# Kernel tuning notes

Measured on AMD Instinct MI355X. Metric: run time of the kernel, lower is better.

The kernel has to match this reference:

```python
import jax, jax.numpy as jnp
import numpy as np

EPS = 1e-5

def _rms(t, w):
    # RMSNorm over last dim with learned scale w (broadcastable)
    return t * jax.lax.rsqrt(jnp.mean(t * t, axis=-1, keepdims=True) + EPS) * w

def setup_inputs() -> dict:
    key = jax.random.key(0)
    ks = jax.random.split(key, 8)
    B, S, D, H, HD, M = 2, 2048, 1024, 16, 64, 2
    E = H * HD
    sc = 0.02
    x = jax.random.normal(ks[0], (B, S, D), jnp.float32)
    attn_mask = jnp.zeros((S, S), jnp.float32)  # additive mask
    mod_ids = jax.random.randint(ks[1], (B, S), 0, M)
    Wq = jax.random.normal(ks[2], (M, D, E), jnp.float32) * sc
    Wk = jax.random.normal(ks[3], (M, D, E), jnp.float32) * sc
    Wv = jax.random.normal(ks[4], (M, D, E), jnp.float32) * sc
    Wo = jax.random.normal(ks[5], (M, E, D), jnp.float32) * sc
    qn_w = jnp.ones((M, HD), jnp.float32)
    kn_w = jnp.ones((M, HD), jnp.float32)
    attn_norm_w = jnp.ones((M, D), jnp.float32)
    return {"x": x, "attn_mask": attn_mask, "mod_ids": mod_ids,
            "Wq": Wq, "Wk": Wk, "Wv": Wv, "Wo": Wo,
            "qn_w": qn_w, "kn_w": kn_w, "attn_norm_w": attn_norm_w}

def reference(x, attn_mask, mod_ids, Wq, Wk, Wv, Wo, qn_w, kn_w, attn_norm_w):
    B, S, D = x.shape
    M = Wq.shape[0]
    HD = qn_w.shape[-1]
    E = Wq.shape[-1]
    H = E // HD
    msk = jax.nn.one_hot(mod_ids, M, dtype=x.dtype)  # [B,S,M] one-hot routing

    # modality-expert QKV projections: [M,B,S,E]
    q_m = jnp.einsum('bsd,mde->mbse', x, Wq).reshape(M, B, S, H, HD)
    k_m = jnp.einsum('bsd,mde->mbse', x, Wk).reshape(M, B, S, H, HD)
    v_m = jnp.einsum('bsd,mde->mbse', x, Wv)
    # per-modality, per-head QK RMSNorm
    q_m = _rms(q_m, qn_w[:, None, None, None, :]).reshape(M, B, S, E)
    k_m = _rms(k_m, kn_w[:, None, None, None, :]).reshape(M, B, S, E)

    # merge modalities (scatter by routing mask)
    q = jnp.einsum('bsm,mbse->bse', msk, q_m).reshape(B, S, H, HD)
    k = jnp.einsum('bsm,mbse->bse', msk, k_m).reshape(B, S, H, HD)
    v = jnp.einsum('bsm,mbse->bse', msk, v_m).reshape(B, S, H, HD)

    # standard multi-head attention
    scores = jnp.einsum('bqhd,bkhd->bhqk', q, k) / jnp.sqrt(jnp.asarray(HD, x.dtype))
    scores = scores + attn_mask  # additive mask broadcast over [B,H]
    attn = jax.nn.softmax(scores, axis=-1)
    ctx = jnp.einsum('bhqk,bkhd->bqhd', attn, v).reshape(B, S, E)
    attn_weights = attn.mean(axis=1)  # [B,S,S], averaged over heads

    # modality-expert output projection + RMSNorm, scatter-merge back
    o_m = jnp.einsum('bse,med->mbsd', ctx, Wo)
    o_m = _rms(o_m, attn_norm_w[:, None, None, :])
    out = jnp.einsum('bsm,mbsd->bsd', msk, o_m)
    return out, attn_weights
```

## Files before the change

kernel.cpp:

```cpp
#include <hip/hip_runtime.h>
#include <cstdint>

#define Bc  2
#define Sc  2048
#define Dc  1024
#define Ec  1024
#define Hc  16
#define HDc 64
#define TTc (Bc*Sc)
#define TILE_R 128
#define NTILES 36
#define EPSc 1e-5f
#define LOG2E 1.44269504f
#define C2    (0.125f*LOG2E)

typedef unsigned short u16;
using bf8   = __attribute__((ext_vector_type(8))) short;
using f32x4 = __attribute__((ext_vector_type(4))) float;
#define MFMA(a,b,c) __builtin_amdgcn_mfma_f32_16x16x32_bf16(a,b,c,0,0,0)

static __device__ __forceinline__ u16 f2b(float f){
    return (u16)((__float_as_uint(f) + 0x8000u) >> 16);
}
static __device__ __forceinline__ float b2f(u16 s){
    return __uint_as_float(((unsigned)s) << 16);
}
static __device__ __forceinline__ unsigned cvtpk(float a, float b){
    unsigned r;
    asm("v_cvt_pk_bf16_f32 %0, %1, %2" : "=v"(r) : "v"(a), "v"(b));
    return r;
}
union bfpack { unsigned u[4]; bf8 v; };
static __device__ __forceinline__ u16* swz(u16* base, int row, int col8){
    return base + row*64 + ((col8 ^ (row & 7)) << 3);
}
static __device__ __forceinline__ const u16* swzc(const u16* base, int row, int col8){
    return base + row*64 + ((col8 ^ (row & 7)) << 3);
}

__global__ void k_perm(const int* __restrict__ mod, int* __restrict__ perm,
                       int* __restrict__ tmeta)
{
    __shared__ int cnt[4], segstart[4];
    int t = threadIdx.x;
    if (t < 4) cnt[t] = 0;
    __syncthreads();
    for (int i = t; i < TTc; i += 256){
        int b = i >> 11; int m = mod[i];
        atomicAdd(&cnt[b*2+m], 1);
    }
    __syncthreads();
    if (t == 0){
        int off = 0;
        for (int i = 0; i < 4; i++){
            segstart[i] = off;
            int pad = ((cnt[i] + TILE_R - 1)/TILE_R)*TILE_R;
            for (int tt = off/TILE_R; tt < (off+pad)/TILE_R; tt++) tmeta[tt] = i;
            off += pad;
        }
        for (int tt = off/TILE_R; tt < NTILES; tt++) tmeta[tt] = -1;
    }
    __syncthreads();
    if (t < 4) cnt[t] = 0;
    for (int i = t; i < NTILES*TILE_R; i += 256) perm[i] = -1;
    __syncthreads();
    for (int i = t; i < TTc; i += 256){
        int b = i >> 11, s = i & 2047; int m = mod[i];
        int r = atomicAdd(&cnt[b*2+m], 1);
        perm[segstart[b*2+m] + r] = s;
    }
}

__global__ __launch_bounds__(256) void k_f2b(const float* __restrict__ src,
                                             u16* __restrict__ dst, int n)
{
    int i = (blockIdx.x*256 + threadIdx.x)*4;
    if (i >= n) return;
    float4 v = *(const float4*)&src[i];
    ushort4 o;
    o.x = f2b(v.x); o.y = f2b(v.y); o.z = f2b(v.z); o.w = f2b(v.w);
    *(ushort4*)&dst[i] = o;
}

__global__ __launch_bounds__(256) void k_f2bs(const float* __restrict__ src,
                                              u16* __restrict__ dst, int n, float sc)
{
    int i = (blockIdx.x*256 + threadIdx.x)*4;
    if (i >= n) return;
    float4 v = *(const float4*)&src[i];
    ushort4 o;
    o.x = f2b(v.x*sc); o.y = f2b(v.y*sc); o.z = f2b(v.z*sc); o.w = f2b(v.w*sc);
    *(ushort4*)&dst[i] = o;
}

__global__ __launch_bounds__(256) void k_tcvt(
    const float* __restrict__ s0, const float* __restrict__ s1,
    const float* __restrict__ s2, const float* __restrict__ s3,
    u16* __restrict__ d0, u16* __restrict__ d1,
    u16* __restrict__ d2, u16* __restrict__ d3)
{
    int wsel = blockIdx.z >> 1, m = blockIdx.z & 1;
    const float* src = (wsel==0?s0:wsel==1?s1:wsel==2?s2:s3) + (size_t)m*1048576;
    u16*       dst = (wsel==0?d0:wsel==1?d1:wsel==2?d2:d3) + (size_t)m*1048576;
    __shared__ float sh[32][33];
    int t = threadIdx.x;
    int i0 = blockIdx.x*32, j0 = blockIdx.y*32;
    {
        int i = t >> 3, j4 = (t & 7)*4;
        *(float4*)&sh[i][j4] = *(const float4*)&src[(size_t)(i0+i)*1024 + j0 + j4];
    }
    __syncthreads();
    {
        int j = t >> 3, i4 = (t & 7)*4;
        ushort4 o;
        o.x = f2b(sh[i4+0][j]); o.y = f2b(sh[i4+1][j]);
        o.z = f2b(sh[i4+2][j]); o.w = f2b(sh[i4+3][j]);
        *(ushort4*)&dst[(size_t)(j0+j)*1024 + i0 + i4] = o;
    }
}

__global__ __launch_bounds__(256) void k_qkv(
    const u16* __restrict__ xb, const u16* __restrict__ wqT,
    const u16* __restrict__ wkT, const u16* __restrict__ wvT,
    const int* __restrict__ perm, const int* __restrict__ tmeta,
    const float* __restrict__ qnw, const float* __restrict__ knw,
    u16* __restrict__ qb, u16* __restrict__ kb, u16* __restrict__ vb)
{
    int meta = tmeta[blockIdx.y];
    if (meta < 0) return;
    int b = meta >> 1, m = meta & 1;
    const u16* W = (blockIdx.z==0 ? wqT : (blockIdx.z==1 ? wkT : wvT)) + (size_t)m*Ec*Dc;
    u16* outp    = (blockIdx.z==0 ? qb  : (blockIdx.z==1 ? kb  : vb));
    int c0 = blockIdx.x*128;
    int t = threadIdx.x, lane = t & 63, wv_ = t >> 6;
    int quad = lane >> 4, lc = lane & 15;

    __shared__ u16 at[128*64];
    __shared__ u16 bt[128*64];
    __shared__ int sperm[128];
    if (t < 128) sperm[t] = perm[blockIdx.y*128 + t];
    f32x4 acc[2][8];
    #pragma unroll
    for (int i=0;i<2;i++)
        #pragma unroll
        for (int j=0;j<8;j++) acc[i][j] = (f32x4){0.f,0.f,0.f,0.f};
    __syncthreads();

    int rr = t >> 1, hf = t & 1;
    for (int d0 = 0; d0 < Dc; d0 += 64){
        int s_ = sperm[rr];
        if (s_ >= 0){
            const u16* src = xb + ((size_t)(b*Sc + s_))*Dc + d0 + hf*32;
            *(uint4*)swz(at, rr, hf*4+0) = *(const uint4*)(src);
            *(uint4*)swz(at, rr, hf*4+1) = *(const uint4*)(src + 8);
            *(uint4*)swz(at, rr, hf*4+2) = *(const uint4*)(src + 16);
            *(uint4*)swz(at, rr, hf*4+3) = *(const uint4*)(src + 24);
        } else {
            uint4 z = make_uint4(0,0,0,0);
            *(uint4*)swz(at, rr, hf*4+0) = z;
            *(uint4*)swz(at, rr, hf*4+1) = z;
            *(uint4*)swz(at, rr, hf*4+2) = z;
            *(uint4*)swz(at, rr, hf*4+3) = z;
        }
        const u16* wsrc = W + (size_t)(c0 + rr)*Dc + d0 + hf*32;
        *(uint4*)swz(bt, rr, hf*4+0) = *(const uint4*)(wsrc);
        *(uint4*)swz(bt, rr, hf*4+1) = *(const uint4*)(wsrc + 8);
        *(uint4*)swz(bt, rr, hf*4+2) = *(const uint4*)(wsrc + 16);
        *(uint4*)swz(bt, rr, hf*4+3) = *(const uint4*)(wsrc + 24);
        __syncthreads();
        #pragma unroll
        for (int ks = 0; ks < 2; ks++){
            bf8 a0 = *(const bf8*)swzc(at, wv_*32 + lc,      ks*4 + quad);
            bf8 a1 = *(const bf8*)swzc(at, wv_*32 + 16 + lc, ks*4 + quad);
            #pragma unroll
            for (int nb = 0; nb < 8; nb++){
                bf8 bb = *(const bf8*)swzc(bt, nb*16 + lc, ks*4 + quad);
                acc[0][nb] = MFMA(a0, bb, acc[0][nb]);
                acc[1][nb] = MFMA(a1, bb, acc[1][nb]);
            }
        }
        __syncthreads();
    }

    if (blockIdx.z < 2){
        const float* nw = (blockIdx.z==0 ? qnw : knw) + m*HDc;
        float cs = (blockIdx.z==0) ? C2 : 1.f;
        float w0 = nw[lc]*cs, w1 = nw[16+lc]*cs, w2 = nw[32+lc]*cs, w3 = nw[48+lc]*cs;
        #pragma unroll
        for (int mb = 0; mb < 2; mb++){
            #pragma unroll
            for (int r = 0; r < 4; r++){
                #pragma unroll
                for (int g = 0; g < 2; g++){
                    float ss = 0.f;
                    #pragma unroll
                    for (int j = 0; j < 4; j++){
                        float v2 = acc[mb][g*4+j][r];
                        ss += v2*v2;
                    }
                    ss += __shfl_xor(ss, 1, 64);
                    ss += __shfl_xor(ss, 2, 64);
                    ss += __shfl_xor(ss, 4, 64);
                    ss += __shfl_xor(ss, 8, 64);
                    float rs = rsqrtf(ss*(1.f/64.f) + EPSc);
                    acc[mb][g*4+0][r] *= rs*w0;
                    acc[mb][g*4+1][r] *= rs*w1;
                    acc[mb][g*4+2][r] *= rs*w2;
                    acc[mb][g*4+3][r] *= rs*w3;
                }
            }
        }
    }

    int h0 = c0 >> 6;
    #pragma unroll
    for (int mb = 0; mb < 2; mb++){
        #pragma unroll
        for (int r = 0; r < 4; r++){
            int row = wv_*32 + mb*16 + quad*4 + r;
            int s_ = sperm[row];
            if (s_ < 0) continue;
            #pragma unroll
            for (int nb = 0; nb < 8; nb++){
                int col = nb*16 + lc;
                int h = h0 + (col >> 6), hd = col & 63;
                outp[(((size_t)(b*Hc + h))*Sc + s_)*HDc + hd] = f2b(acc[mb][nb][r]);
            }
        }
    }
}

__global__ __launch_bounds__(256) void k_vt(const u16* __restrict__ vb,
                                            u16* __restrict__ vtb)
{
    __shared__ u16 sh[64][72];
    int t = threadIdx.x;
    int s0 = blockIdx.x*64, bh = blockIdx.y;
    {
        int rr = t >> 2, cc = (t & 3)*16;
        const u16* src = vb + ((size_t)bh*Sc + s0 + rr)*HDc + cc;
        *(uint4*)&sh[rr][cc]   = *(const uint4*)(src);
        *(uint4*)&sh[rr][cc+8] = *(const uint4*)(src+8);
    }
    __syncthreads();
    {
        int hd = t >> 2, sc = (t & 3)*16;
        u16 tmp[16];
        #pragma unroll
        for (int j = 0; j < 16; j++) tmp[j] = sh[sc+j][hd];
        u16* dst = vtb + ((size_t)bh*HDc + hd)*Sc + s0 + sc;
        *(uint4*)(dst)   = *(const uint4*)&tmp[0];
        *(uint4*)(dst+8) = *(const uint4*)&tmp[8];
    }
}

__global__ __launch_bounds__(256) void k_flash(
    const u16* __restrict__ qb, const u16* __restrict__ kb,
    const u16* __restrict__ vtb, const u16* __restrict__ maskb,
    float* __restrict__ pm, float* __restrict__ pl,
    u16* __restrict__ c0, u16* __restrict__ c1)
{
    int qs0 = blockIdx.x*64, h = blockIdx.y;
    int b = blockIdx.z >> 1, half = blockIdx.z & 1;
    u16* ctxh = half ? c1 : c0;
    int t = threadIdx.x, lane = t & 63, wv_ = t >> 6;
    int quad = lane >> 4, lc = lane & 15;
    __shared__ u16 kt[64*64];
    __shared__ u16 vt[64*64];
    const u16* qp  = qb  + ((size_t)(b*Hc+h))*Sc*HDc;
    const u16* kp  = kb  + ((size_t)(b*Hc+h))*Sc*HDc;
    const u16* vtp = vtb + ((size_t)(b*Hc+h))*HDc*Sc;
    const u16* mq  = maskb + (size_t)(qs0 + wv_*16 + lc)*Sc;
    bf8 aq[2];
    #pragma unroll
    for (int ks = 0; ks < 2; ks++)
        aq[ks] = *(const bf8*)(qp + (size_t)(qs0 + wv_*16 + lc)*HDc + ks*32 + quad*8);
    float rm = -1.0e30f, rl = 0.f;
    f32x4 oacc[4];
    #pragma unroll
    for (int j=0;j<4;j++) oacc[j] = (f32x4){0.f,0.f,0.f,0.f};

    int rr = t >> 2, c8 = (t & 3)*2;
    int pr = (rr & 0x23) | ((rr & 0x04) << 2) | ((rr & 0x18) >> 1);
    int kc0 = half*1024;
    for (int kc = kc0; kc < kc0 + 1024; kc += 64){
        ushort4 mv[2][2];
        #pragma unroll
        for (int a1 = 0; a1 < 2; a1++)
            #pragma unroll
            for (int b1 = 0; b1 < 2; b1++)
                mv[a1][b1] = *(const ushort4*)(mq + kc + a1*32 + quad*8 + b1*4);
        __syncthreads();
        {
            const u16* s1 = kp + (size_t)(kc+rr)*HDc + c8*8;
            *(uint4*)swz(kt, pr, c8)   = *(const uint4*)(s1);
            *(uint4*)swz(kt, pr, c8+1) = *(const uint4*)(s1+8);
            const u16* s2 = vtp + (size_t)rr*Sc + kc + c8*8;
            *(uint4*)swz(vt, rr, c8)   = *(const uint4*)(s2);
            *(uint4*)swz(vt, rr, c8+1) = *(const uint4*)(s2+8);
        }
        __syncthreads();
        f32x4 acc[4];
        #pragma unroll
        for (int j=0;j<4;j++) acc[j] = (f32x4){0.f,0.f,0.f,0.f};
        #pragma unroll
        for (int ks = 0; ks < 2; ks++){
            #pragma unroll
            for (int nb = 0; nb < 4; nb++){
                bf8 ak = *(const bf8*)swzc(kt, nb*16 + lc, ks*4 + quad);
                acc[nb] = MFMA(ak, aq[ks], acc[nb]);
            }
        }
        float sv[4][4];
        float mxl = -3.0e38f;
        #pragma unroll
        for (int a1 = 0; a1 < 2; a1++){
            #pragma unroll
            for (int b1 = 0; b1 < 2; b1++){
                int nb = 2*a1 + b1;
                #pragma unroll
                for (int r = 0; r < 4; r++){
                    u16 mraw = (r==0?mv[a1][b1].x:r==1?mv[a1][b1].y:
                                r==2?mv[a1][b1].z:mv[a1][b1].w);
                    float s2v = acc[nb][r] + b2f(mraw);
                    sv[nb][r] = s2v;
                    mxl = fmaxf(mxl, s2v);
                }
            }
        }
        if (__any(mxl > rm + 8.f)){
            float mx = fmaxf(mxl, __shfl_xor(mxl, 16, 64));
            mx = fmaxf(mx, __shfl_xor(mx, 32, 64));
            float nm = fmaxf(rm, mx);
            float fac = exp2f(rm - nm);
            rm = nm;
            rl *= fac;
            float f0 = __shfl(fac, quad*4+0, 64);
            float f1 = __shfl(fac, quad*4+1, 64);
            float f2 = __shfl(fac, quad*4+2, 64);
            float f3 = __shfl(fac, quad*4+3, 64);
            #pragma unroll
            for (int nb = 0; nb < 4; nb++){
                oacc[nb][0] *= f0; oacc[nb][1] *= f1;
                oacc[nb][2] *= f2; oacc[nb][3] *= f3;
            }
        }
        #pragma unroll
        for (int a1 = 0; a1 < 2; a1++){
            bfpack pk;
            {
                float p0 = exp2f(sv[2*a1][0] - rm);
                float p1 = exp2f(sv[2*a1][1] - rm);
                float p2 = exp2f(sv[2*a1][2] - rm);
                float p3 = exp2f(sv[2*a1][3] - rm);
                rl += (p0 + p1) + (p2 + p3);
                pk.u[0] = cvtpk(p0, p1); pk.u[1] = cvtpk(p2, p3);
            }
            {
                float p0 = exp2f(sv[2*a1+1][0] - rm);
                float p1 = exp2f(sv[2*a1+1][1] - rm);
                float p2 = exp2f(sv[2*a1+1][2] - rm);
                float p3 = exp2f(sv[2*a1+1][3] - rm);
                rl += (p0 + p1) + (p2 + p3);
                pk.u[2] = cvtpk(p0, p1); pk.u[3] = cvtpk(p2, p3);
            }
            bf8 ap = pk.v;
            #pragma unroll
            for (int nb2 = 0; nb2 < 4; nb2++){
                bf8 bv = *(const bf8*)swzc(vt, nb2*16 + lc, a1*4 + quad);
                oacc[nb2] = MFMA(ap, bv, oacc[nb2]);
            }
        }
    }
    rl += __shfl_xor(rl, 16, 64);
    rl += __shfl_xor(rl, 32, 64);
    if (quad == 0){
        size_t srow = ((size_t)(b*Hc+h))*Sc + qs0 + wv_*16 + lc;
        pm[(size_t)half*65536 + srow] = rm;
        pl[(size_t)half*65536 + srow] = rl;
    }
    float i0 = 1.f/__shfl(rl, quad*4+0, 64);
    float i1 = 1.f/__shfl(rl, quad*4+1, 64);
    float i2 = 1.f/__shfl(rl, quad*4+2, 64);
    float i3 = 1.f/__shfl(rl, quad*4+3, 64);
    #pragma unroll
    for (int r = 0; r < 4; r++){
        float ir = (r==0?i0:r==1?i1:r==2?i2:i3);
        int tok = qs0 + wv_*16 + quad*4 + r;
        #pragma unroll
        for (int nb = 0; nb < 4; nb++){
            int hd = nb*16 + lc;
            ctxh[((size_t)(b*Sc + tok))*Ec + h*HDc + hd] = f2b(oacc[nb][r]*ir);
        }
    }
}

__global__ __launch_bounds__(256) void k_merge(
    const float* __restrict__ pm, const float* __restrict__ pl,
    float* __restrict__ lstc, float* __restrict__ w0, float* __restrict__ w1)
{
    int r = blockIdx.x*256 + threadIdx.x;
    float m0 = pm[r],        m1 = pm[65536 + r];
    float l0 = pl[r],        l1 = pl[65536 + r];
    float M  = fmaxf(m0, m1);
    float e0 = exp2f(m0 - M)*l0;
    float e1 = exp2f(m1 - M)*l1;
    float L  = e0 + e1;
    float iL = 1.f/L;
    lstc[r] = M + log2f(L);
    w0[r] = e0*iL;
    w1[r] = e1*iL;
}

__global__ __launch_bounds__(256) void k_addc(u16* __restrict__ c0,
                                              const u16* __restrict__ c1,
                                              const float* __restrict__ w0,
                                              const float* __restrict__ w1)
{
    int i = (blockIdx.x*256 + threadIdx.x)*8;
    int hh = (i >> 6) & 15, s = (i >> 10) & 2047, bb = i >> 21;
    int wi = ((bb*Hc + hh) << 11) + s;
    float wa = w0[wi], wb = w1[wi];
    ushort4 a0 = *(ushort4*)&c0[i],   a1 = *(ushort4*)&c0[i+4];
    ushort4 b0 = *(const ushort4*)&c1[i], b1 = *(const ushort4*)&c1[i+4];
    ushort4 o0, o1;
    o0.x = f2b(b2f(a0.x)*wa + b2f(b0.x)*wb); o0.y = f2b(b2f(a0.y)*wa + b2f(b0.y)*wb);
    o0.z = f2b(b2f(a0.z)*wa + b2f(b0.z)*wb); o0.w = f2b(b2f(a0.w)*wa + b2f(b0.w)*wb);
    o1.x = f2b(b2f(a1.x)*wa + b2f(b1.x)*wb); o1.y = f2b(b2f(a1.y)*wa + b2f(b1.y)*wb);
    o1.z = f2b(b2f(a1.z)*wa + b2f(b1.z)*wb); o1.w = f2b(b2f(a1.w)*wa + b2f(b1.w)*wb);
    *(ushort4*)&c0[i]   = o0;
    *(ushort4*)&c0[i+4] = o1;
}

__global__ __launch_bounds__(256) void k_attnw(
    const u16* __restrict__ qb, const u16* __restrict__ kb,
    const u16* __restrict__ maskb, const float* __restrict__ lstc,
    float* __restrict__ awout)
{
    int qs0 = blockIdx.x*64, ks0 = blockIdx.y*64, b = blockIdx.z;
    int t = threadIdx.x, lane = t & 63, wv_ = t >> 6;
    int quad = lane >> 4, lc = lane & 15;
    __shared__ u16 kt[64*64];
    __shared__ float scc[64];
    f32x4 T[4];
    #pragma unroll
    for (int j=0;j<4;j++) T[j] = (f32x4){0.f,0.f,0.f,0.f};

    for (int h = 0; h < Hc; h++){
        __syncthreads();
        const u16* qp = qb + ((size_t)(b*Hc+h))*Sc*HDc;
        const u16* kp = kb + ((size_t)(b*Hc+h))*Sc*HDc;
        bf8 aq[2];
        #pragma unroll
        for (int ks = 0; ks < 2; ks++)
            aq[ks] = *(const bf8*)(qp + (size_t)(qs0 + wv_*16 + lc)*HDc + ks*32 + quad*8);
        {
            int rr = t >> 2, c8 = (t & 3)*2;
            const u16* s2 = kp + (size_t)(ks0+rr)*HDc + c8*8;
            *(uint4*)swz(kt, rr, c8)   = *(const uint4*)(s2);
            *(uint4*)swz(kt, rr, c8+1) = *(const uint4*)(s2+8);
        }
        if (t < 64)
            scc[t] = lstc[((size_t)(b*Hc+h))*Sc + qs0 + t];
        __syncthreads();
        f32x4 acc[4];
        #pragma unroll
        for (int j=0;j<4;j++) acc[j] = (f32x4){0.f,0.f,0.f,0.f};
        #pragma unroll
        for (int ks = 0; ks < 2; ks++){
            #pragma unroll
            for (int nb = 0; nb < 4; nb++){
                bf8 bb = *(const bf8*)swzc(kt, nb*16 + lc, ks*4 + quad);
                acc[nb] = MFMA(aq[ks], bb, acc[nb]);
            }
        }
        #pragma unroll
        for (int r = 0; r < 4; r++){
            int row = wv_*16 + quad*4 + r;
            float cv = scc[row];
            #pragma unroll
            for (int nb = 0; nb < 4; nb++)
                T[nb][r] += exp2f(acc[nb][r] - cv);
        }
    }
    #pragma unroll
    for (int r = 0; r < 4; r++){
        int gq = qs0 + wv_*16 + quad*4 + r;
        #pragma unroll
        for (int nb = 0; nb < 4; nb++){
            int gk = ks0 + nb*16 + lc;
            float mk = b2f(maskb[(size_t)gq*Sc + gk]);
            awout[(size_t)b*Sc*Sc + (size_t)gq*Sc + gk]
                = T[nb][r]*exp2f(mk)*(1.f/16.f);
        }
    }
}

__global__ __launch_bounds__(256) void k_oproj(
    const u16* __restrict__ ctxb, const u16* __restrict__ woT,
    const int* __restrict__ perm, const int* __restrict__ tmeta,
    float* __restrict__ opre)
{
    int meta = tmeta[blockIdx.y];
    if (meta < 0) return;
    int b = meta >> 1, m = meta & 1;
    const u16* W = woT + (size_t)m*Ec*Dc;
    int c0 = blockIdx.x*128;
    int t = threadIdx.x, lane = t & 63, wv_ = t >> 6;
    int quad = lane >> 4, lc = lane & 15;
    __shared__ u16 at[128*64];
    __shared__ u16 bt[128*64];
    __shared__ int sperm[128];
    if (t < 128) sperm[t] = perm[blockIdx.y*128 + t];
    f32x4 acc[2][8];
    #pragma unroll
    for (int i=0;i<2;i++)
        #pragma unroll
        for (int j=0;j<8;j++) acc[i][j] = (f32x4){0.f,0.f,0.f,0.f};
    __syncthreads();

    int rr = t >> 1, hf = t & 1;
    for (int d0 = 0; d0 < Ec; d0 += 64){
        int s_ = sperm[rr];
        if (s_ >= 0){
            const u16* src = ctxb + ((size_t)(b*Sc + s_))*Ec + d0 + hf*32;
            *(uint4*)swz(at, rr, hf*4+0) = *(const uint4*)(src);
            *(uint4*)swz(at, rr, hf*4+1) = *(const uint4*)(src + 8);
            *(uint4*)swz(at, rr, hf*4+2) = *(const uint4*)(src + 16);
            *(uint4*)swz(at, rr, hf*4+3) = *(const uint4*)(src + 24);
        } else {
            uint4 z = make_uint4(0,0,0,0);
            *(uint4*)swz(at, rr, hf*4+0) = z;
            *(uint4*)swz(at, rr, hf*4+1) = z;
            *(uint4*)swz(at, rr, hf*4+2) = z;
            *(uint4*)swz(at, rr, hf*4+3) = z;
        }
        const u16* wsrc = W + (size_t)(c0 + rr)*Ec + d0 + hf*32;
        *(uint4*)swz(bt, rr, hf*4+0) = *(const uint4*)(wsrc);
        *(uint4*)swz(bt, rr, hf*4+1) = *(const uint4*)(wsrc + 8);
        *(uint4*)swz(bt, rr, hf*4+2) = *(const uint4*)(wsrc + 16);
        *(uint4*)swz(bt, rr, hf*4+3) = *(const uint4*)(wsrc + 24);
        __syncthreads();
        #pragma unroll
        for (int ks = 0; ks < 2; ks++){
            bf8 a0 = *(const bf8*)swzc(at, wv_*32 + lc,      ks*4 + quad);
            bf8 a1 = *(const bf8*)swzc(at, wv_*32 + 16 + lc, ks*4 + quad);
            #pragma unroll
            for (int nb = 0; nb < 8; nb++){
                bf8 bb = *(const bf8*)swzc(bt, nb*16 + lc, ks*4 + quad);
                acc[0][nb] = MFMA(a0, bb, acc[0][nb]);
                acc[1][nb] = MFMA(a1, bb, acc[1][nb]);
            }
        }
        __syncthreads();
    }
    #pragma unroll
    for (int mb = 0; mb < 2; mb++){
        #pragma unroll
        for (int r = 0; r < 4; r++){
            int row = wv_*32 + mb*16 + quad*4 + r;
            int s_ = sperm[row];
            if (s_ < 0) continue;
            #pragma unroll
            for (int nb = 0; nb < 8; nb++){
                int col = c0 + nb*16 + lc;
                opre[((size_t)(b*Sc + s_))*Dc + col] = acc[mb][nb][r];
            }
        }
    }
}

__global__ __launch_bounds__(256) void k_onorm(
    const float* __restrict__ opre, const float* __restrict__ anw,
    const int* __restrict__ mod, float* __restrict__ out)
{
    int row = blockIdx.x;
    int m = mod[row];
    int t = threadIdx.x;
    float val[4];
    float ss = 0.f;
    #pragma unroll
    for (int j=0;j<4;j++){
        val[j] = opre[(size_t)row*Dc + t + 256*j];
        ss += val[j]*val[j];
    }
    #pragma unroll
    for (int o=32;o>0;o>>=1) ss += __shfl_xor(ss, o, 64);
    __shared__ float red[4];
    int wid = t>>6, lane = t&63;
    if (lane==0) red[wid]=ss;
    __syncthreads();
    float tot = red[0]+red[1]+red[2]+red[3];
    float rms = rsqrtf(tot*(1.f/1024.f) + EPSc);
    #pragma unroll
    for (int j=0;j<4;j++)
        out[(size_t)row*Dc + t + 256*j] = val[j]*rms*anw[m*Dc + t + 256*j];
}

extern "C" void kernel_launch(void* const* d_in, const int* in_sizes, int n_in,
                              void* d_out, int out_size, void* d_ws, size_t ws_size,
                              hipStream_t stream)
{
    const float* x    = (const float*)d_in[0];
    const float* mask = (const float*)d_in[1];
    const int*   mod  = (const int*)  d_in[2];
    const float* Wq   = (const float*)d_in[3];
    const float* Wk   = (const float*)d_in[4];
    const float* Wv   = (const float*)d_in[5];
    const float* Wo   = (const float*)d_in[6];
    const float* qnw  = (const float*)d_in[7];
    const float* knw  = (const float*)d_in[8];
    const float* anw  = (const float*)d_in[9];

    float* out   = (float*)d_out;
    float* awout = out + (size_t)Bc*Sc*Dc;

    float* ws = (float*)d_ws;
    u16* qb    = (u16*)(ws + 0);
    u16* kb    = (u16*)(ws + 2097152);
    u16* vb    = (u16*)(ws + 4194304);
    u16* xb    = (u16*)(ws + 6291456);
    u16* ctx0  = xb;
    u16* ctx1  = vb;
    u16* vtb   = (u16*)(ws + 8388608);
    u16* wqT   = (u16*)(ws + 10485760);
    u16* wkT   = (u16*)(ws + 11534336);
    u16* wvT   = (u16*)(ws + 12582912);
    u16* woT   = (u16*)(ws + 13631488);
    float* lstc= ws + 14680064;
    float* pm  = ws + 14811136;
    float* pl  = pm + 131072;
    float* w0  = ws + 15073280;
    float* w1  = w0 + 65536;
    u16* maskb = (u16*)(ws + 15335424);
    int* perm  = (int*)(ws + 17432576);
    int* tmeta = perm + NTILES*TILE_R;
    float* opre = ws;

    k_perm  <<<dim3(1),            256, 0, stream>>>(mod, perm, tmeta);
    k_f2b   <<<dim3(4096),         256, 0, stream>>>(x, xb, Bc*Sc*Dc);
    k_f2bs  <<<dim3(4096),         256, 0, stream>>>(mask, maskb, Sc*Sc, LOG2E);
    k_tcvt  <<<dim3(32,32,8),      256, 0, stream>>>(Wq, Wk, Wv, Wo, wqT, wkT, wvT, woT);
    k_qkv   <<<dim3(8,NTILES,3),   256, 0, stream>>>(xb, wqT, wkT, wvT, perm, tmeta,
                                                     qnw, knw, qb, kb, vb);
    k_vt    <<<dim3(32,32),        256, 0, stream>>>(vb, vtb);
    k_flash <<<dim3(32,16,4),      256, 0, stream>>>(qb, kb, vtb, maskb, pm, pl, ctx0, ctx1);
    k_merge <<<dim3(256),          256, 0, stream>>>(pm, pl, lstc, w0, w1);
    k_attnw <<<dim3(32,32,2),      256, 0, stream>>>(qb, kb, maskb, lstc, awout);
    k_addc  <<<dim3(2048),         256, 0, stream>>>(ctx0, ctx1, w0, w1);
    k_oproj <<<dim3(8,NTILES),     256, 0, stream>>>(ctx0, woT, perm, tmeta, opre);
    k_onorm <<<dim3(4096),         256, 0, stream>>>(opre, anw, mod, out);
}
```

Before: 392.8 us.

## Use direct global-to-LDS loads in GEMMs, read fp32 mask directly, fast exp2

The QKV and output-projection GEMMs now stage A and B tiles with global_load_lds 16-byte transfers that go straight into the swizzled LDS layout. Padded rows point at a small zero buffer that k_perm clears. The separate kernel that converted the mask to bf16 is removed, so flash and attention-weight kernels read the fp32 mask and fold in LOG2E with an fma. exp2f calls become the hardware exp2 builtin. This trims register staging, one kernel launch and a mask pass, at the cost of twice the mask bytes read in the attention kernels.

```diff
diff --git a/kernel.cpp b/kernel.cpp
--- a/kernel.cpp
+++ b/kernel.cpp
@@ -25,6 +25,9 @@
 static __device__ __forceinline__ float b2f(u16 s){
     return __uint_as_float(((unsigned)s) << 16);
 }
+static __device__ __forceinline__ float ex2(float x){
+    return __builtin_amdgcn_exp2f(x);
+}
 static __device__ __forceinline__ unsigned cvtpk(float a, float b){
     unsigned r;
     asm("v_cvt_pk_bf16_f32 %0, %1, %2" : "=v"(r) : "v"(a), "v"(b));
@@ -37,12 +40,18 @@
 static __device__ __forceinline__ const u16* swzc(const u16* base, int row, int col8){
     return base + row*64 + ((col8 ^ (row & 7)) << 3);
 }
+typedef const __attribute__((address_space(1))) void* gp1;
+typedef __attribute__((address_space(3))) void* lp3;
+static __device__ __forceinline__ void gl16(const void* g, void* l){
+    __builtin_amdgcn_global_load_lds((gp1)g, (lp3)l, 16, 0, 0);
+}
 
 __global__ void k_perm(const int* __restrict__ mod, int* __restrict__ perm,
-                       int* __restrict__ tmeta)
+                       int* __restrict__ tmeta, u16* __restrict__ zbuf)
 {
     __shared__ int cnt[4], segstart[4];
     int t = threadIdx.x;
+    for (int i = t; i < 2048; i += 256) zbuf[i] = 0;
     if (t < 4) cnt[t] = 0;
     __syncthreads();
     for (int i = t; i < TTc; i += 256){
@@ -79,17 +88,6 @@
     float4 v = *(const float4*)&src[i];
     ushort4 o;
     o.x = f2b(v.x); o.y = f2b(v.y); o.z = f2b(v.z); o.w = f2b(v.w);
-    *(ushort4*)&dst[i] = o;
-}
-
-__global__ __launch_bounds__(256) void k_f2bs(const float* __restrict__ src,
-                                              u16* __restrict__ dst, int n, float sc)
-{
-    int i = (blockIdx.x*256 + threadIdx.x)*4;
-    if (i >= n) return;
-    float4 v = *(const float4*)&src[i];
-    ushort4 o;
-    o.x = f2b(v.x*sc); o.y = f2b(v.y*sc); o.z = f2b(v.z*sc); o.w = f2b(v.w*sc);
     *(ushort4*)&dst[i] = o;
 }
 
@@ -124,6 +122,7 @@
     const u16* __restrict__ wkT, const u16* __restrict__ wvT,
     const int* __restrict__ perm, const int* __restrict__ tmeta,
     const float* __restrict__ qnw, const float* __restrict__ knw,
+    const u16* __restrict__ zbuf,
     u16* __restrict__ qb, u16* __restrict__ kb, u16* __restrict__ vb)
 {
     int meta = tmeta[blockIdx.y];
@@ -146,27 +145,22 @@
         for (int j=0;j<8;j++) acc[i][j] = (f32x4){0.f,0.f,0.f,0.f};
     __syncthreads();
 
-    int rr = t >> 1, hf = t & 1;
+    int colsw = ((lane & 7) ^ (lane >> 3)) << 3;
+    const u16* ab[4]; const u16* bb[4];
+    #pragma unroll
+    for (int i = 0; i < 4; i++){
+        int row = wv_*32 + i*8 + (lane >> 3);
+        int s_ = sperm[row];
+        ab[i] = (s_ >= 0) ? (xb + ((size_t)(b*Sc + s_))*Dc + colsw) : zbuf;
+        bb[i] = W + (size_t)(c0 + row)*Dc + colsw;
+    }
+
     for (int d0 = 0; d0 < Dc; d0 += 64){
-        int s_ = sperm[rr];
-        if (s_ >= 0){
-            const u16* src = xb + ((size_t)(b*Sc + s_))*Dc + d0 + hf*32;
-            *(uint4*)swz(at, rr, hf*4+0) = *(const uint4*)(src);
-            *(uint4*)swz(at, rr, hf*4+1) = *(const uint4*)(src + 8);
-            *(uint4*)swz(at, rr, hf*4+2) = *(const uint4*)(src + 16);
-            *(uint4*)swz(at, rr, hf*4+3) = *(const uint4*)(src + 24);
-        } else {
-            uint4 z = make_uint4(0,0,0,0);
-            *(uint4*)swz(at, rr, hf*4+0) = z;
-            *(uint4*)swz(at, rr, hf*4+1) = z;
-            *(uint4*)swz(at, rr, hf*4+2) = z;
-            *(uint4*)swz(at, rr, hf*4+3) = z;
-        }
-        const u16* wsrc = W + (size_t)(c0 + rr)*Dc + d0 + hf*32;
-        *(uint4*)swz(bt, rr, hf*4+0) = *(const uint4*)(wsrc);
-        *(uint4*)swz(bt, rr, hf*4+1) = *(const uint4*)(wsrc + 8);
-        *(uint4*)swz(bt, rr, hf*4+2) = *(const uint4*)(wsrc + 16);
-        *(uint4*)swz(bt, rr, hf*4+3) = *(const uint4*)(wsrc + 24);
+        #pragma unroll
+        for (int i = 0; i < 4; i++){
+            gl16(ab[i] + d0, &at[(wv_*4 + i)*512]);
+            gl16(bb[i] + d0, &bt[(wv_*4 + i)*512]);
+        }
         __syncthreads();
         #pragma unroll
         for (int ks = 0; ks < 2; ks++){
@@ -174,9 +168,9 @@
             bf8 a1 = *(const bf8*)swzc(at, wv_*32 + 16 + lc, ks*4 + quad);
             #pragma unroll
             for (int nb = 0; nb < 8; nb++){
-                bf8 bb = *(const bf8*)swzc(bt, nb*16 + lc, ks*4 + quad);
-                acc[0][nb] = MFMA(a0, bb, acc[0][nb]);
-                acc[1][nb] = MFMA(a1, bb, acc[1][nb]);
+                bf8 bb2 = *(const bf8*)swzc(bt, nb*16 + lc, ks*4 + quad);
+                acc[0][nb] = MFMA(a0, bb2, acc[0][nb]);
+                acc[1][nb] = MFMA(a1, bb2, acc[1][nb]);
             }
         }
         __syncthreads();
@@ -256,7 +250,7 @@
 
 __global__ __launch_bounds__(256) void k_flash(
     const u16* __restrict__ qb, const u16* __restrict__ kb,
-    const u16* __restrict__ vtb, const u16* __restrict__ maskb,
+    const u16* __restrict__ vtb, const float* __restrict__ maskf,
     float* __restrict__ pm, float* __restrict__ pl,
     u16* __restrict__ c0, u16* __restrict__ c1)
 {
@@ -270,7 +264,7 @@
     const u16* qp  = qb  + ((size_t)(b*Hc+h))*Sc*HDc;
     const u16* kp  = kb  + ((size_t)(b*Hc+h))*Sc*HDc;
     const u16* vtp = vtb + ((size_t)(b*Hc+h))*HDc*Sc;
-    const u16* mq  = maskb + (size_t)(qs0 + wv_*16 + lc)*Sc;
+    const float* mq = maskf + (size_t)(qs0 + wv_*16 + lc)*Sc;
     bf8 aq[2];
     #pragma unroll
     for (int ks = 0; ks < 2; ks++)
@@ -284,12 +278,12 @@
     int pr = (rr & 0x23) | ((rr & 0x04) << 2) | ((rr & 0x18) >> 1);
     int kc0 = half*1024;
     for (int kc = kc0; kc < kc0 + 1024; kc += 64){
-        ushort4 mv[2][2];
+        float4 mvf[2][2];
         #pragma unroll
         for (int a1 = 0; a1 < 2; a1++)
             #pragma unroll
             for (int b1 = 0; b1 < 2; b1++)
-                mv[a1][b1] = *(const ushort4*)(mq + kc + a1*32 + quad*8 + b1*4);
+                mvf[a1][b1] = *(const float4*)(mq + kc + a1*32 + quad*8 + b1*4);
         __syncthreads();
         {
             const u16* s1 = kp + (size_t)(kc+rr)*HDc + c8*8;
@@ -311,7 +305,7 @@
                 acc[nb] = MFMA(ak, aq[ks], acc[nb]);
             }
         }
-        float sv[4][4];
+        float svv[4][4];
         float mxl = -3.0e38f;
         #pragma unroll
         for (int a1 = 0; a1 < 2; a1++){
@@ -320,10 +314,10 @@
                 int nb = 2*a1 + b1;
                 #pragma unroll
                 for (int r = 0; r < 4; r++){
-                    u16 mraw = (r==0?mv[a1][b1].x:r==1?mv[a1][b1].y:
-                                r==2?mv[a1][b1].z:mv[a1][b1].w);
-                    float s2v = acc[nb][r] + b2f(mraw);
-                    sv[nb][r] = s2v;
+                    float mk = (r==0?mvf[a1][b1].x:r==1?mvf[a1][b1].y:
+                                r==2?mvf[a1][b1].z:mvf[a1][b1].w);
+                    float s2v = fmaf(mk, LOG2E, acc[nb][r]);
+                    svv[nb][r] = s2v;
                     mxl = fmaxf(mxl, s2v);
                 }
             }
@@ -332,7 +326,7 @@
             float mx = fmaxf(mxl, __shfl_xor(mxl, 16, 64));
             mx = fmaxf(mx, __shfl_xor(mx, 32, 64));
             float nm = fmaxf(rm, mx);
-            float fac = exp2f(rm - nm);
+            float fac = ex2(rm - nm);
             rm = nm;
             rl *= fac;
             float f0 = __shfl(fac, quad*4+0, 64);
@@ -349,18 +343,18 @@
         for (int a1 = 0; a1 < 2; a1++){
             bfpack pk;
             {
-                float p0 = exp2f(sv[2*a1][0] - rm);
-                float p1 = exp2f(sv[2*a1][1] - rm);
-                float p2 = exp2f(sv[2*a1][2] - rm);
-                float p3 = exp2f(sv[2*a1][3] - rm);
+                float p0 = ex2(svv[2*a1][0] - rm);
+                float p1 = ex2(svv[2*a1][1] - rm);
+                float p2 = ex2(svv[2*a1][2] - rm);
+                float p3 = ex2(svv[2*a1][3] - rm);
                 rl += (p0 + p1) + (p2 + p3);
                 pk.u[0] = cvtpk(p0, p1); pk.u[1] = cvtpk(p2, p3);
             }
             {
-                float p0 = exp2f(sv[2*a1+1][0] - rm);
-                float p1 = exp2f(sv[2*a1+1][1] - rm);
-                float p2 = exp2f(sv[2*a1+1][2] - rm);
-                float p3 = exp2f(sv[2*a1+1][3] - rm);
+                float p0 = ex2(svv[2*a1+1][0] - rm);
+                float p1 = ex2(svv[2*a1+1][1] - rm);
+                float p2 = ex2(svv[2*a1+1][2] - rm);
+                float p3 = ex2(svv[2*a1+1][3] - rm);
                 rl += (p0 + p1) + (p2 + p3);
                 pk.u[2] = cvtpk(p0, p1); pk.u[3] = cvtpk(p2, p3);
             }
@@ -403,8 +397,8 @@
     float m0 = pm[r],        m1 = pm[65536 + r];
     float l0 = pl[r],        l1 = pl[65536 + r];
     float M  = fmaxf(m0, m1);
-    float e0 = exp2f(m0 - M)*l0;
-    float e1 = exp2f(m1 - M)*l1;
+    float e0 = ex2(m0 - M)*l0;
+    float e1 = ex2(m1 - M)*l1;
     float L  = e0 + e1;
     float iL = 1.f/L;
     lstc[r] = M + log2f(L);
@@ -434,7 +428,7 @@
 
 __global__ __launch_bounds__(256) void k_attnw(
     const u16* __restrict__ qb, const u16* __restrict__ kb,
-    const u16* __restrict__ maskb, const float* __restrict__ lstc,
+    const float* __restrict__ maskf, const float* __restrict__ lstc,
     float* __restrict__ awout)
 {
     int qs0 = blockIdx.x*64, ks0 = blockIdx.y*64, b = blockIdx.z;
@@ -480,7 +474,7 @@
             float cv = scc[row];
             #pragma unroll
             for (int nb = 0; nb < 4; nb++)
-                T[nb][r] += exp2f(acc[nb][r] - cv);
+                T[nb][r] += ex2(acc[nb][r] - cv);
         }
     }
     #pragma unroll
@@ -489,9 +483,9 @@
         #pragma unroll
         for (int nb = 0; nb < 4; nb++){
             int gk = ks0 + nb*16 + lc;
-            float mk = b2f(maskb[(size_t)gq*Sc + gk]);
+            float mk = maskf[(size_t)gq*Sc + gk];
             awout[(size_t)b*Sc*Sc + (size_t)gq*Sc + gk]
-                = T[nb][r]*exp2f(mk)*(1.f/16.f);
+                = T[nb][r]*ex2(mk*LOG2E)*(1.f/16.f);
         }
     }
 }
@@ -499,7 +493,7 @@
 __global__ __launch_bounds__(256) void k_oproj(
     const u16* __restrict__ ctxb, const u16* __restrict__ woT,
     const int* __restrict__ perm, const int* __restrict__ tmeta,
-    float* __restrict__ opre)
+    const u16* __restrict__ zbuf, float* __restrict__ opre)
 {
     int meta = tmeta[blockIdx.y];
     if (meta < 0) return;
@@ -519,27 +513,22 @@
         for (int j=0;j<8;j++) acc[i][j] = (f32x4){0.f,0.f,0.f,0.f};
     __syncthreads();
 
-    int rr = t >> 1, hf = t & 1;
+    int colsw = ((lane & 7) ^ (lane >> 3)) << 3;
+    const u16* ab[4]; const u16* bb[4];
+    #pragma unroll
+    for (int i = 0; i < 4; i++){
+        int row = wv_*32 + i*8 + (lane >> 3);
+        int s_ = sperm[row];
+        ab[i] = (s_ >= 0) ? (ctxb + ((size_t)(b*Sc + s_))*Ec + colsw) : zbuf;
+        bb[i] = W + (size_t)(c0 + row)*Ec + colsw;
+    }
+
     for (int d0 = 0; d0 < Ec; d0 += 64){
-        int s_ = sperm[rr];
-        if (s_ >= 0){
-            const u16* src = ctxb + ((size_t)(b*Sc + s_))*Ec + d0 + hf*32;
-            *(uint4*)swz(at, rr, hf*4+0) = *(const uint4*)(src);
-            *(uint4*)swz(at, rr, hf*4+1) = *(const uint4*)(src + 8);
-            *(uint4*)swz(at, rr, hf*4+2) = *(const uint4*)(src + 16);
-            *(uint4*)swz(at, rr, hf*4+3) = *(const uint4*)(src + 24);
-        } else {
-            uint4 z = make_uint4(0,0,0,0);
-            *(uint4*)swz(at, rr, hf*4+0) = z;
-            *(uint4*)swz(at, rr, hf*4+1) = z;
-            *(uint4*)swz(at, rr, hf*4+2) = z;
-            *(uint4*)swz(at, rr, hf*4+3) = z;
-        }
-        const u16* wsrc = W + (size_t)(c0 + rr)*Ec + d0 + hf*32;
-        *(uint4*)swz(bt, rr, hf*4+0) = *(const uint4*)(wsrc);
-        *(uint4*)swz(bt, rr, hf*4+1) = *(const uint4*)(wsrc + 8);
-        *(uint4*)swz(bt, rr, hf*4+2) = *(const uint4*)(wsrc + 16);
-        *(uint4*)swz(bt, rr, hf*4+3) = *(const uint4*)(wsrc + 24);
+        #pragma unroll
+        for (int i = 0; i < 4; i++){
+            gl16(ab[i] + d0, &at[(wv_*4 + i)*512]);
+            gl16(bb[i] + d0, &bt[(wv_*4 + i)*512]);
+        }
         __syncthreads();
         #pragma unroll
         for (int ks = 0; ks < 2; ks++){
@@ -547,9 +536,9 @@
             bf8 a1 = *(const bf8*)swzc(at, wv_*32 + 16 + lc, ks*4 + quad);
             #pragma unroll
             for (int nb = 0; nb < 8; nb++){
-                bf8 bb = *(const bf8*)swzc(bt, nb*16 + lc, ks*4 + quad);
-                acc[0][nb] = MFMA(a0, bb, acc[0][nb]);
-                acc[1][nb] = MFMA(a1, bb, acc[1][nb]);
+                bf8 bb2 = *(const bf8*)swzc(bt, nb*16 + lc, ks*4 + quad);
+                acc[0][nb] = MFMA(a0, bb2, acc[0][nb]);
+                acc[1][nb] = MFMA(a1, bb2, acc[1][nb]);
             }
         }
         __syncthreads();
@@ -632,22 +621,21 @@
     float* pl  = pm + 131072;
     float* w0  = ws + 15073280;
     float* w1  = w0 + 65536;
-    u16* maskb = (u16*)(ws + 15335424);
     int* perm  = (int*)(ws + 17432576);
     int* tmeta = perm + NTILES*TILE_R;
+    u16* zbuf  = (u16*)(tmeta + NTILES + 28);
     float* opre = ws;
 
-    k_perm  <<<dim3(1),            256, 0, stream>>>(mod, perm, tmeta);
+    k_perm  <<<dim3(1),            256, 0, stream>>>(mod, perm, tmeta, zbuf);
     k_f2b   <<<dim3(4096),         256, 0, stream>>>(x, xb, Bc*Sc*Dc);
-    k_f2bs  <<<dim3(4096),         256, 0, stream>>>(mask, maskb, Sc*Sc, LOG2E);
     k_tcvt  <<<dim3(32,32,8),      256, 0, stream>>>(Wq, Wk, Wv, Wo, wqT, wkT, wvT, woT);
     k_qkv   <<<dim3(8,NTILES,3),   256, 0, stream>>>(xb, wqT, wkT, wvT, perm, tmeta,
-                                                     qnw, knw, qb, kb, vb);
+                                                     qnw, knw, zbuf, qb, kb, vb);
     k_vt    <<<dim3(32,32),        256, 0, stream>>>(vb, vtb);
-    k_flash <<<dim3(32,16,4),      256, 0, stream>>>(qb, kb, vtb, maskb, pm, pl, ctx0, ctx1);
+    k_flash <<<dim3(32,16,4),      256, 0, stream>>>(qb, kb, vtb, mask, pm, pl, ctx0, ctx1);
     k_merge <<<dim3(256),          256, 0, stream>>>(pm, pl, lstc, w0, w1);
-    k_attnw <<<dim3(32,32,2),      256, 0, stream>>>(qb, kb, maskb, lstc, awout);
+    k_attnw <<<dim3(32,32,2),      256, 0, stream>>>(qb, kb, mask, lstc, awout);
     k_addc  <<<dim3(2048),         256, 0, stream>>>(ctx0, ctx1, w0, w1);
-    k_oproj <<<dim3(8,NTILES),     256, 0, stream>>>(ctx0, woT, perm, tmeta, opre);
+    k_oproj <<<dim3(8,NTILES),     256, 0, stream>>>(ctx0, woT, perm, tmeta, zbuf, opre);
     k_onorm <<<dim3(4096),         256, 0, stream>>>(opre, anw, mod, out);
 }
```

New measurement: 371.5 us. -5.4%, faster.
